# Optimization experiments

Measured on AMD Instinct MI355X. Metric: run time of the kernel, lower is better.

The kernel has to match this reference:

```python
import jax, jax.numpy as jnp
import numpy as np

N_NODES = 50000


def setup_inputs() -> dict:
    key = jax.random.key(0)
    k_x, k_e, k_w1, k_w2 = jax.random.split(key, 4)
    in_c, hid, out_c = 256, 128, 64
    x = jax.random.normal(k_x, (N_NODES, in_c), dtype=jnp.float32)
    edge_index = jax.random.randint(k_e, (2, 800000), 0, N_NODES, dtype=jnp.int64)
    # Glorot-ish scaled weights (faithful to GCNConv default init scale)
    W1 = jax.random.normal(k_w1, (in_c, hid), dtype=jnp.float32) * (1.0 / np.sqrt(in_c))
    b1 = jnp.zeros((hid,), dtype=jnp.float32)
    W2 = jax.random.normal(k_w2, (hid, out_c), dtype=jnp.float32) * (1.0 / np.sqrt(hid))
    b2 = jnp.zeros((out_c,), dtype=jnp.float32)
    return {"x": x, "edge_index": edge_index, "W1": W1, "b1": b1, "W2": W2, "b2": b2}


def _gcn_norm(edge_index, n_nodes):
    # Add self loops, compute symmetric normalization D^-1/2 A D^-1/2.
    loop = jnp.arange(n_nodes, dtype=edge_index.dtype)
    src = jnp.concatenate([edge_index[0], loop])
    dst = jnp.concatenate([edge_index[1], loop])
    deg = jax.ops.segment_sum(jnp.ones_like(dst, dtype=jnp.float32), dst,
                              num_segments=n_nodes)
    dis = jnp.where(deg > 0, jax.lax.rsqrt(deg), 0.0)  # deg_inv_sqrt
    norm = dis[src] * dis[dst]  # [E + N]
    return src, dst, norm


def _gcn_conv(x, W, b, src, dst, norm, n_nodes):
    h = x @ W                                  # [N, F_out] dense transform first
    msgs = h[src] * norm[:, None]              # edge-wise gather + scale
    agg = jax.ops.segment_sum(msgs, dst, num_segments=n_nodes)  # scatter-add
    return agg + b


def reference(x, edge_index, W1, b1, W2, b2):
    n = x.shape[0]
    src, dst, norm = _gcn_norm(edge_index, n)  # cached=True: same norm both layers
    h = _gcn_conv(x, W1, b1, src, dst, norm, n)
    h = jax.nn.relu(h)
    # Dropout is identity in eval mode (deterministic reference)
    return _gcn_conv(h, W2, b2, src, dst, norm, n)
```

## Files before the change

kernel.cpp:

```cpp
#include <hip/hip_runtime.h>


#define IN_C 256
#define HID 128
#define OUTC 64
#define NBLK 128

typedef __attribute__((ext_vector_type(8))) short short8;
typedef __attribute__((ext_vector_type(4))) float f32x4;

__device__ __forceinline__ void gload_lds16(const void* src, void* dst) {
    __builtin_amdgcn_global_load_lds(
        (const __attribute__((address_space(1))) unsigned int*)src,
        (__attribute__((address_space(3))) unsigned int*)dst, 16, 0, 0);
}

__device__ __forceinline__ void bf16split(float f, ushort& h, ushort& l) {
    unsigned u = __float_as_uint(f);
    h = (ushort)(u >> 16);
    float hf = __uint_as_float(u & 0xFFFF0000u);
    unsigned v = __float_as_uint(f - hf);
    l = (ushort)((v + 0x7FFF + ((v >> 16) & 1)) >> 16);
}

__device__ __forceinline__ void cvt8(float4 f0, float4 f1, short8& hi8, short8& lo8) {
    float ff[8];
    *(float4*)&ff[0] = f0; *(float4*)&ff[4] = f1;
    unsigned* hp = (unsigned*)&hi8;
    unsigned* lp = (unsigned*)&lo8;
    #pragma unroll
    for (int i = 0; i < 4; ++i) {
        unsigned u0 = __float_as_uint(ff[2 * i]), u1 = __float_as_uint(ff[2 * i + 1]);
        unsigned hf0 = u0 & 0xFFFF0000u, hf1 = u1 & 0xFFFF0000u;
        hp[i] = (u0 >> 16) | hf1;
        float r0 = ff[2 * i]     - __uint_as_float(hf0);
        float r1 = ff[2 * i + 1] - __uint_as_float(hf1);
        lp[i] = (__float_as_uint(r0) >> 16) | (__float_as_uint(r1) & 0xFFFF0000u);
    }
}

__device__ __forceinline__ ushort f2bf(float f) {
    unsigned u = __float_as_uint(f);
    return (ushort)((u + 0x7FFF + ((u >> 16) & 1)) >> 16);
}
__device__ __forceinline__ float bf2f(ushort u) {
    return __uint_as_float((unsigned)u << 16);
}

__device__ __forceinline__ int edge_at(const void* ei, long long idx, int is32) {
    return is32 ? ((const int*)ei)[idx] : (int)((const long long*)ei)[idx];
}

__global__ void detect_kernel(const unsigned long long* ei, int* flag) {
    if (threadIdx.x == 0 && blockIdx.x == 0) {
        int is32 = 0;
        for (int i = 0; i < 64; ++i)
            if (ei[i] >> 32) { is32 = 1; break; }
        *flag = is32;
    }
}

__global__ __launch_bounds__(256) void wtrans_kernel(const float* __restrict__ W1,
                                                     const float* __restrict__ W2,
                                                     ushort* __restrict__ wf1,
                                                     ushort* __restrict__ wf2) {
    int id = blockIdx.x * 256 + threadIdx.x;
    if (id < 8192) {
        int lane = id & 63, r = id >> 6;
        int pl = r & 1, nt = (r >> 1) & 7, kidx = r >> 4;
        int n = nt * 16 + (lane & 15);
        int kb = kidx * 32 + (lane >> 4) * 8;
        ushort v[8];
        #pragma unroll
        for (int j = 0; j < 8; ++j) {
            ushort h, l; bf16split(W1[(kb + j) * HID + n], h, l);
            v[j] = pl ? l : h;
        }
        *(short8*)&wf1[(size_t)id * 8] = *(short8*)v;
    } else if (id < 10240) {
        int id2 = id - 8192;
        int lane = id2 & 63, r = id2 >> 6;
        int pl = r & 1, nt = (r >> 1) & 3, kidx = r >> 3;
        int n = nt * 16 + (lane & 15);
        int kb = kidx * 32 + (lane >> 4) * 8;
        ushort v[8];
        #pragma unroll
        for (int j = 0; j < 8; ++j) {
            ushort h, l; bf16split(W2[(kb + j) * OUTC + n], h, l);
            v[j] = pl ? l : h;
        }
        *(short8*)&wf2[(size_t)id2 * 8] = *(short8*)v;
    }
}

__global__ __launch_bounds__(256) void bin_count(const void* ei, const int* __restrict__ flag,
                                                 int* __restrict__ blkcnt, int E, int nb) {
    __shared__ int h[256];
    int t = threadIdx.x;
    h[t] = 0;
    __syncthreads();
    int is32 = *flag;
    int chunk = (E + gridDim.x - 1) / gridDim.x;
    long long s0 = (long long)blockIdx.x * chunk;
    long long s1 = s0 + chunk; if (s1 > E) s1 = E;
    for (long long e = s0 + t; e < s1; e += 256) {
        int d = edge_at(ei, (long long)E + e, is32);
        atomicAdd(&h[d >> 8], 1);
    }
    __syncthreads();
    if (t < nb) blkcnt[t * NBLK + blockIdx.x] = h[t];
}

__global__ __launch_bounds__(256) void bin_scan(int* __restrict__ blkcnt,
                                                int* __restrict__ bbase, int nb) {
    __shared__ int sh[256];
    int t = threadIdx.x;
    int tot = 0;
    if (t < nb) {
        int4* p = (int4*)&blkcnt[t * NBLK];
        int run = 0;
        for (int i = 0; i < NBLK / 4; ++i) {
            int4 v = p[i]; int4 o;
            o.x = run; run += v.x; o.y = run; run += v.y;
            o.z = run; run += v.z; o.w = run; run += v.w;
            p[i] = o;
        }
        tot = run;
    }
    sh[t] = tot;
    __syncthreads();
    for (int d = 1; d < 256; d <<= 1) {
        int add = (t >= d) ? sh[t - d] : 0;
        __syncthreads();
        sh[t] += add;
        __syncthreads();
    }
    if (t < nb) {
        bbase[t] = sh[t] - tot;
        if (t == nb - 1) bbase[nb] = sh[t];
    }
}

__global__ __launch_bounds__(256) void bin_scatter(const void* ei, const int* __restrict__ flag,
                                                   const int* __restrict__ blkcnt,
                                                   const int* __restrict__ bbase,
                                                   unsigned* __restrict__ coarse, int E, int nb) {
    __shared__ int cur[256];
    int t = threadIdx.x;
    if (t < nb) cur[t] = bbase[t] + blkcnt[t * NBLK + blockIdx.x];
    __syncthreads();
    int is32 = *flag;
    int chunk = (E + gridDim.x - 1) / gridDim.x;
    long long s0 = (long long)blockIdx.x * chunk;
    long long s1 = s0 + chunk; if (s1 > E) s1 = E;
    for (long long e = s0 + t; e < s1; e += 256) {
        int s = edge_at(ei, e, is32);
        int d = edge_at(ei, (long long)E + e, is32);
        int p = atomicAdd(&cur[d >> 8], 1);
        coarse[p] = (unsigned)s | ((unsigned)(d & 255) << 17);
    }
}

__global__ __launch_bounds__(256) void fine_kernel(const unsigned* __restrict__ coarse,
                                                   const int* __restrict__ bbase,
                                                   int* __restrict__ row_ptr,
                                                   float* __restrict__ dis,
                                                   int* __restrict__ epk, int N, int nb) {
    __shared__ int h[256], cur[256], sh[256];
    int b = blockIdx.x, t = threadIdx.x;
    int nb0 = b << 8;
    int e0b = bbase[b], e1b = bbase[b + 1];
    h[t] = 0;
    __syncthreads();
    for (int e = e0b + t; e < e1b; e += 256)
        atomicAdd(&h[(coarse[e] >> 17) & 0xFF], 1);
    __syncthreads();
    int cnt = h[t];
    sh[t] = cnt;
    __syncthreads();
    for (int d = 1; d < 256; d <<= 1) {
        int add = (t >= d) ? sh[t - d] : 0;
        __syncthreads();
        sh[t] += add;
        __syncthreads();
    }
    int excl = sh[t] - cnt;
    int node = nb0 + t;
    if (node < N) {
        row_ptr[node] = e0b + excl;
        dis[node] = rsqrtf((float)cnt + 1.0f);
        if (node == N - 1) row_ptr[N] = e0b + sh[t];
    }
    cur[t] = e0b + excl;
    __syncthreads();
    for (int e = e0b + t; e < e1b; e += 256) {
        unsigned r = coarse[e];
        int p = atomicAdd(&cur[(r >> 17) & 0xFF], 1);
        epk[p] = (int)(r & 0x1FFFF);
    }
}

__global__ void zsent_kernel(ushort* h1, ushort* h2) {
    int t = threadIdx.x;
    if (t < 128) h1[t] = 0;
    if (t < 64)  h2[t] = 0;
}

__global__ __launch_bounds__(256) void gemm1_mfma(const float* __restrict__ X,
                                                  const ushort* __restrict__ wf1,
                                                  const float* __restrict__ dis,
                                                  ushort* __restrict__ HB, int N) {
    __shared__ float xs[64 * 64];
    int t = threadIdx.x;
    int lane = t & 63, w = t >> 6;
    int m_off = (w >> 1) * 32, n_off = (w & 1) * 64;
    long long row0 = (long long)blockIdx.x * 64;
    f32x4 acc[2][4] = {};
    for (int k0i = 0; k0i < 4; ++k0i) {
        __syncthreads();
        #pragma unroll
        for (int i = 0; i < 4; ++i) {
            int lrow = w * 16 + i * 4 + (lane >> 4);
            long long gr = row0 + lrow; if (gr >= N) gr = N - 1;
            int gchunk = (lane & 15) ^ (lrow & 7);
            gload_lds16(X + gr * IN_C + k0i * 64 + gchunk * 4,
                        xs + (w * 16 + i * 4) * 64);
        }
        __syncthreads();
        #pragma unroll
        for (int kk = 0; kk < 2; ++kk) {
            int kidx = k0i * 2 + kk;
            short8 ah[2], al[2], bh[4], bl[4];
            #pragma unroll
            for (int ni = 0; ni < 4; ++ni) {
                int nt = (n_off >> 4) + ni;
                const ushort* bp = wf1 + (size_t)(kidx * 16 + nt * 2) * 512 + lane * 8;
                bh[ni] = *(const short8*)bp;
                bl[ni] = *(const short8*)(bp + 512);
            }
            #pragma unroll
            for (int mi = 0; mi < 2; ++mi) {
                int r = m_off + mi * 16 + (lane & 15);
                int s = r & 7;
                int c0 = kk * 8 + (lane >> 4) * 2;
                float4 f0 = *(float4*)((char*)xs + r * 256 + ((c0 ^ s) * 16));
                float4 f1 = *(float4*)((char*)xs + r * 256 + (((c0 + 1) ^ s) * 16));
                cvt8(f0, f1, ah[mi], al[mi]);
            }
            #pragma unroll
            for (int mi = 0; mi < 2; ++mi)
                #pragma unroll
                for (int ni = 0; ni < 4; ++ni) {
                    acc[mi][ni] = __builtin_amdgcn_mfma_f32_16x16x32_bf16(ah[mi], bh[ni], acc[mi][ni], 0, 0, 0);
                    acc[mi][ni] = __builtin_amdgcn_mfma_f32_16x16x32_bf16(ah[mi], bl[ni], acc[mi][ni], 0, 0, 0);
                    acc[mi][ni] = __builtin_amdgcn_mfma_f32_16x16x32_bf16(al[mi], bh[ni], acc[mi][ni], 0, 0, 0);
                }
        }
    }
    int cr = (lane >> 4) * 4, cc = lane & 15;
    #pragma unroll
    for (int mi = 0; mi < 2; ++mi)
        #pragma unroll
        for (int j = 0; j < 4; ++j) {
            long long gr = row0 + m_off + mi * 16 + cr + j;
            if (gr < N) {
                float dv = dis[gr];
                #pragma unroll
                for (int ni = 0; ni < 4; ++ni) {
                    int col = n_off + ni * 16 + cc;
                    HB[gr * HID + col] = f2bf(acc[mi][ni][j] * dv);
                }
            }
        }
}

__global__ __launch_bounds__(256) void gemm2_mfma(const ushort* __restrict__ Ah,
                                                  const ushort* __restrict__ Al,
                                                  const ushort* __restrict__ wf2,
                                                  const float* __restrict__ dis,
                                                  ushort* __restrict__ HB, int N) {
    __shared__ ushort ash[64 * 64], asl[64 * 64];
    int t = threadIdx.x;
    int lane = t & 63, w = t >> 6;
    int m_off = (w >> 1) * 32, n_off = (w & 1) * 32;
    long long row0 = (long long)blockIdx.x * 64;
    f32x4 acc[2][2] = {};
    for (int k0i = 0; k0i < 2; ++k0i) {
        __syncthreads();
        #pragma unroll
        for (int i = 0; i < 2; ++i) {
            int rbase = w * 16 + i * 8;
            long long gr = row0 + rbase + (lane >> 3);
            size_t so = (size_t)gr * 128 + k0i * 64 + (lane & 7) * 8;
            gload_lds16(Ah + so, ash + rbase * 64);
            gload_lds16(Al + so, asl + rbase * 64);
        }
        __syncthreads();
        #pragma unroll
        for (int kk = 0; kk < 2; ++kk) {
            int kidx = k0i * 2 + kk;
            short8 ah[2], al[2], bh[2], bl[2];
            #pragma unroll
            for (int ni = 0; ni < 2; ++ni) {
                int nt = (n_off >> 4) + ni;
                const ushort* bp = wf2 + (size_t)(kidx * 8 + nt * 2) * 512 + lane * 8;
                bh[ni] = *(const short8*)bp;
                bl[ni] = *(const short8*)(bp + 512);
            }
            #pragma unroll
            for (int mi = 0; mi < 2; ++mi) {
                int r = m_off + mi * 16 + (lane & 15);
                int pos = (kk * 4 + (lane >> 4)) ^ (r & 7);
                ah[mi] = *(short8*)((char*)ash + r * 128 + pos * 16);
                al[mi] = *(short8*)((char*)asl + r * 128 + pos * 16);
            }
            #pragma unroll
            for (int mi = 0; mi < 2; ++mi)
                #pragma unroll
                for (int ni = 0; ni < 2; ++ni) {
                    acc[mi][ni] = __builtin_amdgcn_mfma_f32_16x16x32_bf16(ah[mi], bh[ni], acc[mi][ni], 0, 0, 0);
                    acc[mi][ni] = __builtin_amdgcn_mfma_f32_16x16x32_bf16(ah[mi], bl[ni], acc[mi][ni], 0, 0, 0);
                    acc[mi][ni] = __builtin_amdgcn_mfma_f32_16x16x32_bf16(al[mi], bh[ni], acc[mi][ni], 0, 0, 0);
                }
        }
    }
    int cr = (lane >> 4) * 4, cc = lane & 15;
    #pragma unroll
    for (int mi = 0; mi < 2; ++mi)
        #pragma unroll
        for (int j = 0; j < 4; ++j) {
            long long gr = row0 + m_off + mi * 16 + cr + j;
            if (gr < N) {
                float dv = dis[gr];
                #pragma unroll
                for (int ni = 0; ni < 2; ++ni)
                    HB[gr * OUTC + n_off + ni * 16 + cc] = f2bf(acc[mi][ni][j] * dv);
            }
        }
}

template <int MODE>
__global__ __launch_bounds__(256) void seg_agg_v8(const ushort* __restrict__ H,
                                                  const float* __restrict__ dis,
                                                  const int* __restrict__ row_ptr,
                                                  const int* __restrict__ epk,
                                                  const float* __restrict__ bias,
                                                  float* __restrict__ outF,
                                                  ushort* __restrict__ outH,
                                                  ushort* __restrict__ outL,
                                                  int N) {
    int lane = threadIdx.x & 63;
    int node = (int)(((long long)blockIdx.x * blockDim.x + threadIdx.x) >> 6);
    if (node >= N) return;
    int e0 = row_ptr[node], e1 = row_ptr[node + 1];
    if constexpr (MODE == 0) {
        const unsigned* hl = (const unsigned*)H + lane;
        unsigned v = hl[node * 64];
        float a0 = bf2f((ushort)v), a1 = bf2f((ushort)(v >> 16));
        for (int base = e0; base < e1; base += 64) {
            int cnt = min(64, e1 - base);
            int rec = epk[min(base + lane, e1 - 1)];
            for (int u0 = 0; u0 < cnt; u0 += 16) {
                unsigned hv[16];
                #pragma unroll
                for (int u = 0; u < 16; ++u) {
                    int s = (u0 + u < cnt) ? __builtin_amdgcn_readlane(rec, u0 + u) : N;
                    hv[u] = hl[s * 64];
                }
                #pragma unroll
                for (int u = 0; u < 16; ++u) {
                    a0 += bf2f((ushort)hv[u]);
                    a1 += bf2f((ushort)(hv[u] >> 16));
                }
            }
        }
        float dn = dis[node];
        int c0 = lane * 2;
        float2 bb = *(const float2*)&bias[c0];
        float p0 = fmaxf(dn * a0 + bb.x, 0.f);
        float p1 = fmaxf(dn * a1 + bb.y, 0.f);
        unsigned u0b = __float_as_uint(p0), u1b = __float_as_uint(p1);
        unsigned h0 = u0b >> 16, h1 = u1b >> 16;
        float r0 = p0 - __uint_as_float(u0b & 0xFFFF0000u);
        float r1 = p1 - __uint_as_float(u1b & 0xFFFF0000u);
        unsigned l0 = __float_as_uint(r0) >> 16, l1 = __float_as_uint(r1) >> 16;
        int sl = c0 >> 6, e = c0 & 63;
        int ch = ((e >> 3) ^ (node & 7));
        size_t pos = (size_t)node * 128 + sl * 64 + ch * 8 + (e & 7);
        *(unsigned*)&outH[pos] = h0 | (h1 << 16);
        *(unsigned*)&outL[pos] = l0 | (l1 << 16);
    } else {
        const ushort* hl = H + lane;
        float acc = bf2f(hl[node * 64]);
        for (int base = e0; base < e1; base += 64) {
            int cnt = min(64, e1 - base);
            int rec = epk[min(base + lane, e1 - 1)];
            for (int u0 = 0; u0 < cnt; u0 += 16) {
                float hv[16];
                #pragma unroll
                for (int u = 0; u < 16; ++u) {
                    int s = (u0 + u < cnt) ? __builtin_amdgcn_readlane(rec, u0 + u) : N;
                    hv[u] = bf2f(hl[s * 64]);
                }
                #pragma unroll
                for (int u = 0; u < 16; ++u)
                    acc += hv[u];
            }
        }
        outF[(size_t)node * 64 + lane] = dis[node] * acc + bias[lane];
    }
}

extern "C" void kernel_launch(void* const* d_in, const int* in_sizes, int n_in,
                              void* d_out, int out_size, void* d_ws, size_t ws_size,
                              hipStream_t stream) {
    const float* x  = (const float*)d_in[0];
    const void*  ei = d_in[1];
    const float* W1 = (const float*)d_in[2];
    const float* b1 = (const float*)d_in[3];
    const float* W2 = (const float*)d_in[4];
    const float* b2 = (const float*)d_in[5];
    float* out = (float*)d_out;
    int N = in_sizes[0] / IN_C;
    int E = in_sizes[1] / 2;
    int nb = (N + 255) >> 8;
    int nblk64 = (N + 63) / 64;
    int N_pad = nblk64 * 64;

    char* ws = (char*)d_ws;
    size_t off = 0;
    auto alloc = [&](size_t bytes) {
        void* p = ws + off;
        off += ((bytes + 255) / 256) * 256;
        return p;
    };
    int*      flag    = (int*)alloc(4);
    int*      blkcnt  = (int*)alloc((size_t)nb * NBLK * 4);
    int*      bbase   = (int*)alloc(((size_t)nb + 1) * 4);
    int*      row_ptr = (int*)alloc(((size_t)N + 1) * 4);
    float*    dis     = (float*)alloc((size_t)N * 4);
    unsigned* coarse  = (unsigned*)alloc((size_t)E * 4);
    int*      epk     = (int*)alloc((size_t)E * 4);
    ushort*   wf1     = (ushort*)alloc(131072);
    ushort*   wf2     = (ushort*)alloc(32768);
    ushort*   H1b     = (ushort*)alloc(((size_t)N + 1) * HID * 2);
    ushort*   Ah      = (ushort*)alloc((size_t)N_pad * 128 * 2);
    ushort*   Al      = (ushort*)alloc((size_t)N_pad * 128 * 2);
    ushort*   H2b     = (ushort*)alloc(((size_t)N + 1) * OUTC * 2);

    detect_kernel<<<1, 64, 0, stream>>>((const unsigned long long*)ei, flag);
    wtrans_kernel<<<40, 256, 0, stream>>>(W1, W2, wf1, wf2);
    bin_count<<<NBLK, 256, 0, stream>>>(ei, flag, blkcnt, E, nb);
    bin_scan<<<1, 256, 0, stream>>>(blkcnt, bbase, nb);
    bin_scatter<<<NBLK, 256, 0, stream>>>(ei, flag, blkcnt, bbase, coarse, E, nb);
    fine_kernel<<<nb, 256, 0, stream>>>(coarse, bbase, row_ptr, dis, epk, N, nb);
    zsent_kernel<<<1, 128, 0, stream>>>(H1b + (size_t)N * HID, H2b + (size_t)N * OUTC);
    gemm1_mfma<<<nblk64, 256, 0, stream>>>(x, wf1, dis, H1b, N);

    int agg_blocks = (int)(((long long)N * 64 + 255) / 256);
    seg_agg_v8<0><<<agg_blocks, 256, 0, stream>>>(H1b, dis, row_ptr, epk,
                                                  b1, nullptr, Ah, Al, N);
    gemm2_mfma<<<nblk64, 256, 0, stream>>>(Ah, Al, wf2, dis, H2b, N);
    seg_agg_v8<1><<<agg_blocks, 256, 0, stream>>>(H2b, dis, row_ptr, epk,
                                                  b2, out, nullptr, nullptr, N);
}
```

Before: 142.1 us.

## Fold tiny kernels away, double binning blocks, sub-sort CSR edges by source quartile

Drops the separate detect and zero-sentinel launches: the index-width check is inlined into the binning kernels and the sentinel rows are zeroed by wtrans_kernel. NBLK doubles so the coarse binning passes launch more blocks. fine_kernel now also orders each destination's edge list by source-node quartile, so the later gather over H rows touches nearby source rows together and should get better cache locality. The costs are more shared-memory histogram work in fine_kernel and a redundant 64-element detection read in every block.

```diff
diff --git a/kernel.cpp b/kernel.cpp
--- a/kernel.cpp
+++ b/kernel.cpp
@@ -4,7 +4,7 @@
 #define IN_C 256
 #define HID 128
 #define OUTC 64
-#define NBLK 128
+#define NBLK 256
 
 typedef __attribute__((ext_vector_type(8))) short short8;
 typedef __attribute__((ext_vector_type(4))) float f32x4;
@@ -51,19 +51,20 @@
     return is32 ? ((const int*)ei)[idx] : (int)((const long long*)ei)[idx];
 }
 
-__global__ void detect_kernel(const unsigned long long* ei, int* flag) {
-    if (threadIdx.x == 0 && blockIdx.x == 0) {
-        int is32 = 0;
-        for (int i = 0; i < 64; ++i)
-            if (ei[i] >> 32) { is32 = 1; break; }
-        *flag = is32;
-    }
+__device__ __forceinline__ int detect32(const void* ei) {
+    const unsigned long long* p = (const unsigned long long*)ei;
+    int is32 = 0;
+    for (int i = 0; i < 64; ++i)
+        if (p[i] >> 32) { is32 = 1; break; }
+    return is32;
 }
 
 __global__ __launch_bounds__(256) void wtrans_kernel(const float* __restrict__ W1,
                                                      const float* __restrict__ W2,
                                                      ushort* __restrict__ wf1,
-                                                     ushort* __restrict__ wf2) {
+                                                     ushort* __restrict__ wf2,
+                                                     ushort* __restrict__ h1sent,
+                                                     ushort* __restrict__ h2sent) {
     int id = blockIdx.x * 256 + threadIdx.x;
     if (id < 8192) {
         int lane = id & 63, r = id >> 6;
@@ -90,16 +91,22 @@
             v[j] = pl ? l : h;
         }
         *(short8*)&wf2[(size_t)id2 * 8] = *(short8*)v;
-    }
-}
-
-__global__ __launch_bounds__(256) void bin_count(const void* ei, const int* __restrict__ flag,
+    } else if (id < 10368) {
+        h1sent[id - 10240] = 0;
+    } else if (id < 10432) {
+        h2sent[id - 10368] = 0;
+    }
+}
+
+__global__ __launch_bounds__(256) void bin_count(const void* ei,
                                                  int* __restrict__ blkcnt, int E, int nb) {
     __shared__ int h[256];
+    __shared__ int s_is32;
     int t = threadIdx.x;
     h[t] = 0;
-    __syncthreads();
-    int is32 = *flag;
+    if (t == 0) s_is32 = detect32(ei);
+    __syncthreads();
+    int is32 = s_is32;
     int chunk = (E + gridDim.x - 1) / gridDim.x;
     long long s0 = (long long)blockIdx.x * chunk;
     long long s1 = s0 + chunk; if (s1 > E) s1 = E;
@@ -141,15 +148,17 @@
     }
 }
 
-__global__ __launch_bounds__(256) void bin_scatter(const void* ei, const int* __restrict__ flag,
+__global__ __launch_bounds__(256) void bin_scatter(const void* ei,
                                                    const int* __restrict__ blkcnt,
                                                    const int* __restrict__ bbase,
                                                    unsigned* __restrict__ coarse, int E, int nb) {
     __shared__ int cur[256];
+    __shared__ int s_is32;
     int t = threadIdx.x;
     if (t < nb) cur[t] = bbase[t] + blkcnt[t * NBLK + blockIdx.x];
-    __syncthreads();
-    int is32 = *flag;
+    if (t == 0) s_is32 = detect32(ei);
+    __syncthreads();
+    int is32 = s_is32;
     int chunk = (E + gridDim.x - 1) / gridDim.x;
     long long s0 = (long long)blockIdx.x * chunk;
     long long s1 = s0 + chunk; if (s1 > E) s1 = E;
@@ -165,45 +174,51 @@
                                                    const int* __restrict__ bbase,
                                                    int* __restrict__ row_ptr,
                                                    float* __restrict__ dis,
-                                                   int* __restrict__ epk, int N, int nb) {
-    __shared__ int h[256], cur[256], sh[256];
+                                                   int* __restrict__ epk,
+                                                   int N, int nb, int q1, int q2, int q3) {
+    __shared__ int h[1024], cur[1024], ssum[256];
     int b = blockIdx.x, t = threadIdx.x;
     int nb0 = b << 8;
     int e0b = bbase[b], e1b = bbase[b + 1];
-    h[t] = 0;
-    __syncthreads();
-    for (int e = e0b + t; e < e1b; e += 256)
-        atomicAdd(&h[(coarse[e] >> 17) & 0xFF], 1);
-    __syncthreads();
-    int cnt = h[t];
-    sh[t] = cnt;
+    #pragma unroll
+    for (int i = 0; i < 4; ++i) h[t + i * 256] = 0;
+    __syncthreads();
+    for (int e = e0b + t; e < e1b; e += 256) {
+        unsigned r = coarse[e];
+        int sv = (int)(r & 0x1FFFF);
+        int qq = (sv >= q2) ? (sv >= q3 ? 3 : 2) : (sv >= q1 ? 1 : 0);
+        atomicAdd(&h[(((r >> 17) & 0xFF) << 2) | qq], 1);
+    }
+    __syncthreads();
+    int v0 = h[4 * t], v1 = h[4 * t + 1], v2 = h[4 * t + 2], v3 = h[4 * t + 3];
+    int s = v0 + v1 + v2 + v3;
+    ssum[t] = s;
     __syncthreads();
     for (int d = 1; d < 256; d <<= 1) {
-        int add = (t >= d) ? sh[t - d] : 0;
-        __syncthreads();
-        sh[t] += add;
-        __syncthreads();
-    }
-    int excl = sh[t] - cnt;
+        int add = (t >= d) ? ssum[t - d] : 0;
+        __syncthreads();
+        ssum[t] += add;
+        __syncthreads();
+    }
+    int excl = ssum[t] - s;
     int node = nb0 + t;
     if (node < N) {
         row_ptr[node] = e0b + excl;
-        dis[node] = rsqrtf((float)cnt + 1.0f);
-        if (node == N - 1) row_ptr[N] = e0b + sh[t];
-    }
-    cur[t] = e0b + excl;
+        dis[node] = rsqrtf((float)s + 1.0f);
+        if (node == N - 1) row_ptr[N] = e0b + ssum[t];
+    }
+    cur[4 * t] = e0b + excl;
+    cur[4 * t + 1] = e0b + excl + v0;
+    cur[4 * t + 2] = e0b + excl + v0 + v1;
+    cur[4 * t + 3] = e0b + excl + v0 + v1 + v2;
     __syncthreads();
     for (int e = e0b + t; e < e1b; e += 256) {
         unsigned r = coarse[e];
-        int p = atomicAdd(&cur[(r >> 17) & 0xFF], 1);
-        epk[p] = (int)(r & 0x1FFFF);
-    }
-}
-
-__global__ void zsent_kernel(ushort* h1, ushort* h2) {
-    int t = threadIdx.x;
-    if (t < 128) h1[t] = 0;
-    if (t < 64)  h2[t] = 0;
+        int sv = (int)(r & 0x1FFFF);
+        int qq = (sv >= q2) ? (sv >= q3 ? 3 : 2) : (sv >= q1 ? 1 : 0);
+        int p = atomicAdd(&cur[(((r >> 17) & 0xFF) << 2) | qq], 1);
+        epk[p] = sv;
+    }
 }
 
 __global__ __launch_bounds__(256) void gemm1_mfma(const float* __restrict__ X,
@@ -434,7 +449,6 @@
         off += ((bytes + 255) / 256) * 256;
         return p;
     };
-    int*      flag    = (int*)alloc(4);
     int*      blkcnt  = (int*)alloc((size_t)nb * NBLK * 4);
     int*      bbase   = (int*)alloc(((size_t)nb + 1) * 4);
     int*      row_ptr = (int*)alloc(((size_t)N + 1) * 4);
@@ -448,13 +462,14 @@
     ushort*   Al      = (ushort*)alloc((size_t)N_pad * 128 * 2);
     ushort*   H2b     = (ushort*)alloc(((size_t)N + 1) * OUTC * 2);
 
-    detect_kernel<<<1, 64, 0, stream>>>((const unsigned long long*)ei, flag);
-    wtrans_kernel<<<40, 256, 0, stream>>>(W1, W2, wf1, wf2);
-    bin_count<<<NBLK, 256, 0, stream>>>(ei, flag, blkcnt, E, nb);
+    wtrans_kernel<<<41, 256, 0, stream>>>(W1, W2, wf1, wf2,
+                                          H1b + (size_t)N * HID,
+                                          H2b + (size_t)N * OUTC);
+    bin_count<<<NBLK, 256, 0, stream>>>(ei, blkcnt, E, nb);
     bin_scan<<<1, 256, 0, stream>>>(blkcnt, bbase, nb);
-    bin_scatter<<<NBLK, 256, 0, stream>>>(ei, flag, blkcnt, bbase, coarse, E, nb);
-    fine_kernel<<<nb, 256, 0, stream>>>(coarse, bbase, row_ptr, dis, epk, N, nb);
-    zsent_kernel<<<1, 128, 0, stream>>>(H1b + (size_t)N * HID, H2b + (size_t)N * OUTC);
+    bin_scatter<<<NBLK, 256, 0, stream>>>(ei, blkcnt, bbase, coarse, E, nb);
+    fine_kernel<<<nb, 256, 0, stream>>>(coarse, bbase, row_ptr, dis, epk,
+                                        N, nb, N / 4, N / 2, (3 * N) / 4);
     gemm1_mfma<<<nblk64, 256, 0, stream>>>(x, wf1, dis, H1b, N);
 
     int agg_blocks = (int)(((long long)N * 64 + 255) / 256);
```

Measured after the change: 140.0 us. No clear change (-1.4%).
